# Kernel optimization log

Measured on AMD Instinct MI355X. Metric: run time of the kernel, lower is better.

The kernel has to match this reference:

```python
import jax, jax.numpy as jnp
import numpy as np

NUM_HEADS = 12
HEAD_SIZE = 64
HIDDEN = NUM_HEADS * HEAD_SIZE  # 768
ONE_SIDED_WINDOW = 256          # attention_window 512 // 2
NEG = -10000.0


def setup_inputs() -> dict:
    key = jax.random.key(0)
    ks = jax.random.split(key, 16)
    B, W, E, H = 1, 2048, 128, HIDDEN
    std = 0.02
    def lin(kw, kb):
        return (jax.random.normal(kw, (H, H), jnp.float32) * std,
                jax.random.normal(kb, (H,), jnp.float32) * std)
    q_w, q_b = lin(ks[0], ks[1])
    k_w, k_b = lin(ks[2], ks[3])
    v_w, v_b = lin(ks[4], ks[5])
    w2e_w, w2e_b = lin(ks[6], ks[7])
    e2w_w, e2w_b = lin(ks[8], ks[9])
    e2e_w, e2e_b = lin(ks[10], ks[11])
    return {
        "word_hidden_states": jax.random.normal(ks[12], (B, W, H), jnp.float32),
        "entity_hidden_states": jax.random.normal(ks[13], (B, E, H), jnp.float32),
        "attention_mask": jnp.zeros((B, 1, 1, W + E), jnp.float32),
        "q_w": q_w, "q_b": q_b, "k_w": k_w, "k_b": k_b, "v_w": v_w, "v_b": v_b,
        "w2e_w": w2e_w, "w2e_b": w2e_b, "e2w_w": e2w_w, "e2w_b": e2w_b,
        "e2e_w": e2e_w, "e2e_b": e2e_b,
    }


def reference(word_hidden_states, entity_hidden_states, attention_mask,
              q_w, q_b, k_w, k_b, v_w, v_b,
              w2e_w, w2e_b, e2w_w, e2w_b, e2e_w, e2e_b):
    B, W, H = word_hidden_states.shape
    E = entity_hidden_states.shape[1]
    S = W + E

    def heads(x):  # [B, L, H] -> [B, nh, L, hd]
        return x.reshape(B, -1, NUM_HEADS, HEAD_SIZE).transpose(0, 2, 1, 3)

    concat = jnp.concatenate([word_hidden_states, entity_hidden_states], axis=1)
    k = heads(concat @ k_w + k_b)          # [B, nh, S, hd]
    v = heads(concat @ v_w + v_b)
    q_w2w = heads(word_hidden_states @ q_w + q_b)
    q_w2e = heads(word_hidden_states @ w2e_w + w2e_b)
    q_e2w = heads(entity_hidden_states @ e2w_w + e2w_b)
    q_e2e = heads(entity_hidden_states @ e2e_w + e2e_b)

    k_word, k_ent = k[:, :, :W], k[:, :, W:]

    # --- w2w: Longformer sliding-window QK^T, then _conversion to a dense
    # [B, nh, W, W] matrix with out-of-band entries set to -10000. ---
    w2w = jnp.einsum('bhid,bhjd->bhij', q_w2w, k_word)  # [B, nh, W, W]
    idx = jnp.arange(W)
    in_band = jnp.abs(idx[:, None] - idx[None, :]) <= ONE_SIDED_WINDOW  # [W, W]
    # diagonal mask: float_mask[j] (-10000 where attention_mask != 0) added
    # within the band (broadcast over heads / query positions)
    mask_words = attention_mask[:, 0, 0, :W]                # [B, W]
    float_mask = jnp.where(mask_words != 0.0, NEG, 0.0)     # [B, W]
    w2w = w2w + float_mask[:, None, None, :]
    # _conversion: out-of-band -> -10000; also exact zeros -> -10000 (source quirk)
    w2w = jnp.where(in_band[None, None] & (w2w != 0.0), w2w, NEG)

    # --- entity-aware dense blocks ---
    w2e = jnp.einsum('bhid,bhjd->bhij', q_w2e, k_ent)    # [B, nh, W, E]
    e2w = jnp.einsum('bhid,bhjd->bhij', q_e2w, k_word)   # [B, nh, E, W]
    e2e = jnp.einsum('bhid,bhjd->bhij', q_e2e, k_ent)    # [B, nh, E, E]

    word_scores = jnp.concatenate([w2w, w2e], axis=3)    # [B, nh, W, S]
    ent_scores = jnp.concatenate([e2w, e2e], axis=3)     # [B, nh, E, S]
    scores = jnp.concatenate([word_scores, ent_scores], axis=2)  # [B, nh, S, S]

    scores = scores / jnp.sqrt(jnp.float32(HEAD_SIZE)) + attention_mask
    probs = jax.nn.softmax(scores, axis=-1)

    ctx = jnp.einsum('bhij,bhjd->bhid', probs, v)        # [B, nh, S, hd]
    ctx = ctx.transpose(0, 2, 1, 3).reshape(B, S, H)
    return ctx[:, :W, :], ctx[:, W:, :]
```

## Files before the change

kernel.cpp:

```cpp
#include <hip/hip_runtime.h>

typedef __bf16 bf16x8 __attribute__((ext_vector_type(8)));
typedef unsigned short u16x8 __attribute__((ext_vector_type(8)));
typedef u16x8 u16x8_a __attribute__((may_alias));
typedef unsigned int u32x2 __attribute__((ext_vector_type(2)));
typedef u32x2 u32x2_a __attribute__((may_alias));
typedef unsigned int u32x4 __attribute__((ext_vector_type(4)));
typedef u32x4 u32x4_a __attribute__((may_alias));
typedef float f32x4 __attribute__((ext_vector_type(4)));
typedef float f32x16 __attribute__((ext_vector_type(16)));

#define LOG2E 1.4426950408889634f
#define NEGV  -10000.0f

__device__ __forceinline__ unsigned int cvtpk(float lo, float hi){
  unsigned int r;
  asm("v_cvt_pk_bf16_f32 %0, %1, %2" : "=v"(r) : "v"(lo), "v"(hi));
  return r;
}
__device__ __forceinline__ bf16x8 ldb(const unsigned short* p){
  return __builtin_bit_cast(bf16x8, *(const u16x8_a*)p);
}
__device__ __forceinline__ bf16x8 mkfrag(unsigned a, unsigned b, unsigned c, unsigned d){
  u32x4 v = {a,b,c,d};
  return __builtin_bit_cast(bf16x8, v);
}
__device__ __forceinline__ void gload16(const unsigned short* g, unsigned short* l){
  __builtin_amdgcn_global_load_lds(
    (const __attribute__((address_space(1))) void*)g,
    (__attribute__((address_space(3))) void*)l, 16, 0, 0);
}

__global__ __launch_bounds__(256) void prep(
    const float* __restrict__ w0, const float* __restrict__ w1,
    const float* __restrict__ w2, const float* __restrict__ w3,
    const float* __restrict__ w4, const float* __restrict__ w5,
    const float* __restrict__ word, const float* __restrict__ ent,
    const float* __restrict__ am,
    unsigned short* __restrict__ outT, unsigned short* __restrict__ Abf,
    float* __restrict__ amT, float* __restrict__ negT)
{
  int z = blockIdx.z, tid = threadIdx.x;
  if (z == 6){
    size_t id = (size_t)blockIdx.y*24 + blockIdx.x;
    size_t e = (id*256 + tid)*8;
    const size_t WE = (size_t)2048*768;
    const float* s = (e < WE) ? (word + e) : (ent + (e - WE));
    float4 a = *(const float4*)s;
    float4 b = *(const float4*)(s+4);
    u32x4 v = {cvtpk(a.x,a.y), cvtpk(a.z,a.w), cvtpk(b.x,b.y), cvtpk(b.z,b.w)};
    *(u32x4_a*)(Abf + e) = v;
    return;
  }
  if (z == 7){
    if (blockIdx.y != 0 || blockIdx.x >= 9) return;
    int j = blockIdx.x*256 + tid;
    if (j < 2176){
      float a = am[j];
      amT[j]  = a * LOG2E;
      negT[j] = (a != 0.f) ? NEGV : 0.f;
    }
    return;
  }
  if (blockIdx.y >= 24) return;
  const float* src;
  switch (z){
    case 0: src = w0; break; case 1: src = w1; break; case 2: src = w2; break;
    case 3: src = w3; break; case 4: src = w4; break; default: src = w5; break;
  }
  unsigned short* dst = outT + (size_t)z * 589824;
  __shared__ float tile[32][33];
  int tx = tid & 31, ty = tid >> 5;
  int x0 = blockIdx.x*32, y0 = blockIdx.y*32;
  #pragma unroll
  for (int i=0;i<32;i+=8) tile[ty+i][tx] = src[(size_t)(y0+ty+i)*768 + x0+tx];
  __syncthreads();
  #pragma unroll
  for (int i=0;i<32;i+=16){
    unsigned int u = cvtpk(tile[tx][ty+i], tile[tx][ty+i+8]);
    dst[(size_t)(x0+ty+i)*768 + y0+tx]   = (unsigned short)u;
    dst[(size_t)(x0+ty+i+8)*768 + y0+tx] = (unsigned short)(u>>16);
  }
}

__global__ __launch_bounds__(256) void gemm_proj(
    const unsigned short* __restrict__ Abf,
    const unsigned short* __restrict__ wT,
    const float* __restrict__ bK, const float* __restrict__ bV,
    const float* __restrict__ bQ, const float* __restrict__ bWE,
    const float* __restrict__ bEW, const float* __restrict__ bEE,
    unsigned short* __restrict__ oK, unsigned short* __restrict__ VbT,
    unsigned short* __restrict__ oQ, unsigned short* __restrict__ oWE,
    unsigned short* __restrict__ oEW, unsigned short* __restrict__ oEE)
{
  int mt = blockIdx.x, ntile = blockIdx.y;
  int g, mg;
  if      (mt < 17){ g=0; mg=mt;    }
  else if (mt < 34){ g=1; mg=mt-17; }
  else if (mt < 50){ g=2; mg=mt-34; }
  else if (mt < 66){ g=3; mg=mt-50; }
  else if (mt < 67){ g=4; mg=0;     }
  else             { g=5; mg=0;     }
  int m0 = mg*128;
  const unsigned short* A = Abf + (size_t)((g>=4 ? 2048 : 0) + m0)*768;
  const unsigned short* B = wT + (size_t)g*589824;
  const float* bias; unsigned short* out;
  switch (g){
    case 0: bias=bK;  out=oK;  break;
    case 1: bias=bV;  out=0;   break;
    case 2: bias=bQ;  out=oQ;  break;
    case 3: bias=bWE; out=oWE; break;
    case 4: bias=bEW; out=oEW; break;
    default:bias=bEE; out=oEE; break;
  }
  int n0 = ntile*128;

  __shared__ __align__(16) unsigned short a_s[128*32];
  __shared__ __align__(16) unsigned short b_s[128*32];

  int tid  = threadIdx.x;
  int w    = tid>>6, lane = tid&63, quad = lane>>4, lr = lane&15;
  int wm   = (w&1)*64, wn = (w>>1)*64;

  f32x4 acc[4][4];
  #pragma unroll
  for (int i=0;i<4;i++) for (int j=0;j<4;j++) for (int r=0;r<4;r++) acc[i][j][r]=0.f;

  int srow = lane>>2;
  int scol = (lane&3)*8;
  const unsigned short* gA0 = A + (size_t)(w*32 + srow)*768 + scol;
  const unsigned short* gA1 = gA0 + (size_t)16*768;
  const unsigned short* gB0 = B + (size_t)(n0 + w*32 + srow)*768 + scol;
  const unsigned short* gB1 = gB0 + (size_t)16*768;
  unsigned short* lA0 = a_s + w*32*32;
  unsigned short* lA1 = lA0 + 16*32;
  unsigned short* lB0 = b_s + w*32*32;
  unsigned short* lB1 = lB0 + 16*32;

  for (int k0=0; k0<768; k0+=32){
    __syncthreads();
    gload16(gA0 + k0, lA0);
    gload16(gA1 + k0, lA1);
    gload16(gB0 + k0, lB0);
    gload16(gB1 + k0, lB1);
    __syncthreads();
    bf16x8 af[4], bfr[4];
    #pragma unroll
    for (int i=0;i<4;i++) af[i]  = ldb(a_s + (wm+i*16+lr)*32 + quad*8);
    #pragma unroll
    for (int j=0;j<4;j++) bfr[j] = ldb(b_s + (wn+j*16+lr)*32 + quad*8);
    #pragma unroll
    for (int i=0;i<4;i++)
      #pragma unroll
      for (int j=0;j<4;j++)
        acc[i][j] = __builtin_amdgcn_mfma_f32_16x16x32_bf16(af[i], bfr[j], acc[i][j], 0,0,0);
  }
  if (g == 1){
    #pragma unroll
    for (int j=0;j<4;j++){
      int col = n0 + wn + j*16 + lr;
      float bb = bias[col];
      #pragma unroll
      for (int i=0;i<4;i++){
        int rowb = m0 + wm + i*16 + quad*4;
        u32x2 uv = {cvtpk(acc[i][j][0]+bb, acc[i][j][1]+bb),
                    cvtpk(acc[i][j][2]+bb, acc[i][j][3]+bb)};
        *(u32x2_a*)(VbT + (size_t)col*2176 + rowb) = uv;
      }
    }
  } else {
    out += (size_t)m0*768;
    #pragma unroll
    for (int j=0;j<4;j++){
      int col = n0 + wn + j*16 + lr;
      float bb = bias[col];
      #pragma unroll
      for (int i=0;i<4;i++){
        int rowb = wm + i*16 + quad*4;
        unsigned int u01 = cvtpk(acc[i][j][0]+bb, acc[i][j][1]+bb);
        unsigned int u23 = cvtpk(acc[i][j][2]+bb, acc[i][j][3]+bb);
        out[(size_t)(rowb+0)*768 + col] = (unsigned short)u01;
        out[(size_t)(rowb+1)*768 + col] = (unsigned short)(u01>>16);
        out[(size_t)(rowb+2)*768 + col] = (unsigned short)u23;
        out[(size_t)(rowb+3)*768 + col] = (unsigned short)(u23>>16);
      }
    }
  }
}

__global__ __launch_bounds__(256) void attn_split(
  const unsigned short* __restrict__ Kb,  const unsigned short* __restrict__ VbT,
  const unsigned short* __restrict__ Qw,  const unsigned short* __restrict__ Qwe,
  const unsigned short* __restrict__ Qew, const unsigned short* __restrict__ Qee,
  const float* __restrict__ amT, const float* __restrict__ negT,
  float* __restrict__ outw, float* __restrict__ pO, float* __restrict__ pML)
{
  int lin = blockIdx.x + 80*blockIdx.y;
  int wid = (lin & 7)*120 + (lin >> 3);
  int bx = wid % 80;
  int h  = wid / 80;

  int tid = threadIdx.x, w = tid>>6, lane = tid&63;
  int l31 = lane & 31, hi = lane >> 5;
  int hi8 = hi*8, hi4 = hi*4;
  bool isword = bx < 64;
  int qrb, eg=0, eq=0;
  const unsigned short *Qa, *Qb;
  if (isword){ qrb = bx*32; Qa=Qw;  Qb=Qwe; }
  else       { int e = bx-64; eg = e>>2; eq = e&3; qrb = eg*32; Qa=Qew; Qb=Qee; }
  int hofs = h*64;

  __shared__ float part[4][64][35];

  const unsigned short* qr = Qa + (size_t)(qrb+l31)*768 + hofs + hi8;
  bf16x8 qa0 = ldb(qr), qa1 = ldb(qr+16), qa2 = ldb(qr+32), qa3 = ldb(qr+48);
  qr = Qb + (size_t)(qrb+l31)*768 + hofs + hi8;
  bf16x8 qb0 = ldb(qr), qb1 = ldb(qr+16), qb2 = ldb(qr+32), qb3 = ldb(qr+48);

  float m = -1e30f, l = 0.f;
  f32x16 o0, o1;
  #pragma unroll
  for (int r=0;r<16;r++){ o0[r] = 0.f; o1[r] = 0.f; }

  int lo, nw, start, end;
  if (isword){
    lo = qrb - 256; if (lo < 0) lo = 0;
    int hiq = qrb + 288; if (hiq > 2048) hiq = 2048;
    nw = (hiq - lo) >> 5;
    start = w; end = nw + 4;
  } else {
    lo = 0; nw = 64;
    start = eq*17 + w; end = eq*17 + 17;
  }
  int iq = qrb + l31;

  for (int c = start; c < end; c += 4){
    bool entp = c >= nw;
    int j0 = entp ? (2048 + (c-nw)*32) : (lo + c*32);

    const unsigned short* kp = Kb + (size_t)(j0+l31)*768 + hofs + hi8;
    bf16x8 ka0 = ldb(kp), ka1 = ldb(kp+16), ka2 = ldb(kp+32), ka3 = ldb(kp+48);
    const unsigned short* vp = VbT + (size_t)(hofs + l31)*2176 + j0 + hi8;
    bf16x8 va00 = ldb(vp),           va01 = ldb(vp + 16);
    bf16x8 va10 = ldb(vp + 32*2176), va11 = ldb(vp + 32*2176 + 16);
    float4 aT0 = *(const float4*)(amT + j0 + hi4);
    float4 aT1 = *(const float4*)(amT + j0 + 8  + hi4);
    float4 aT2 = *(const float4*)(amT + j0 + 16 + hi4);
    float4 aT3 = *(const float4*)(amT + j0 + 24 + hi4);

    bf16x8 qf0 = entp ? qb0 : qa0, qf1 = entp ? qb1 : qa1;
    bf16x8 qf2 = entp ? qb2 : qa2, qf3 = entp ? qb3 : qa3;

    f32x16 s;
    #pragma unroll
    for (int r=0;r<16;r++) s[r] = 0.f;
    __builtin_amdgcn_s_setprio(1);
    s = __builtin_amdgcn_mfma_f32_32x32x16_bf16(ka0, qf0, s, 0,0,0);
    s = __builtin_amdgcn_mfma_f32_32x32x16_bf16(ka1, qf1, s, 0,0,0);
    s = __builtin_amdgcn_mfma_f32_32x32x16_bf16(ka2, qf2, s, 0,0,0);
    s = __builtin_amdgcn_mfma_f32_32x32x16_bf16(ka3, qf3, s, 0,0,0);
    __builtin_amdgcn_s_setprio(0);

    float sc[16];
    if (isword && !entp){
      float4 nT0 = *(const float4*)(negT + j0 + hi4);
      float4 nT1 = *(const float4*)(negT + j0 + 8  + hi4);
      float4 nT2 = *(const float4*)(negT + j0 + 16 + hi4);
      float4 nT3 = *(const float4*)(negT + j0 + 24 + hi4);
      int djb = iq + 256 - (j0 + hi4);
      #pragma unroll
      for (int e=0;e<4;e++){
        { float sv = s[e]    + nT0[e];
          bool ok = ((unsigned)(djb - e)      <= 512u) && (sv != 0.f);
          sc[e]    = (ok ? sv : NEGV) * (LOG2E*0.125f) + aT0[e]; }
        { float sv = s[4+e]  + nT1[e];
          bool ok = ((unsigned)(djb - 8 - e)  <= 512u) && (sv != 0.f);
          sc[4+e]  = (ok ? sv : NEGV) * (LOG2E*0.125f) + aT1[e]; }
        { float sv = s[8+e]  + nT2[e];
          bool ok = ((unsigned)(djb - 16 - e) <= 512u) && (sv != 0.f);
          sc[8+e]  = (ok ? sv : NEGV) * (LOG2E*0.125f) + aT2[e]; }
        { float sv = s[12+e] + nT3[e];
          bool ok = ((unsigned)(djb - 24 - e) <= 512u) && (sv != 0.f);
          sc[12+e] = (ok ? sv : NEGV) * (LOG2E*0.125f) + aT3[e]; }
      }
    } else {
      #pragma unroll
      for (int e=0;e<4;e++){
        sc[e]    = s[e]    * (LOG2E*0.125f) + aT0[e];
        sc[4+e]  = s[4+e]  * (LOG2E*0.125f) + aT1[e];
        sc[8+e]  = s[8+e]  * (LOG2E*0.125f) + aT2[e];
        sc[12+e] = s[12+e] * (LOG2E*0.125f) + aT3[e];
      }
    }

    float mx = sc[0];
    #pragma unroll
    for (int r=1;r<16;r++) mx = fmaxf(mx, sc[r]);
    mx = fmaxf(mx, __shfl_xor(mx, 32));

    float mn;
    if (__all(mx <= m)){
      mn = m;
    } else {
      mn = fmaxf(m, mx);
      float alpha = exp2f(m - mn);
      m = mn;
      l *= alpha;
      #pragma unroll
      for (int r=0;r<16;r++){ o0[r] *= alpha; o1[r] *= alpha; }
    }

    float p[16];
    #pragma unroll
    for (int r=0;r<16;r++) p[r] = exp2f(sc[r]-mn);

    float rs = ((p[0]+p[1])+(p[2]+p[3])) + ((p[4]+p[5])+(p[6]+p[7]))
             + ((p[8]+p[9])+(p[10]+p[11])) + ((p[12]+p[13])+(p[14]+p[15]));
    rs += __shfl_xor(rs, 32);
    l += rs;

    unsigned pk0 = cvtpk(p[0], p[1]),  pk1 = cvtpk(p[2], p[3]);
    unsigned pk2 = cvtpk(p[4], p[5]),  pk3 = cvtpk(p[6], p[7]);
    unsigned pk4 = cvtpk(p[8], p[9]),  pk5 = cvtpk(p[10], p[11]);
    unsigned pk6 = cvtpk(p[12], p[13]),pk7 = cvtpk(p[14], p[15]);

    bool hib = hi != 0;
    unsigned t0 = hib ? pk0 : pk2;
    unsigned t1 = hib ? pk1 : pk3;
    unsigned t2 = hib ? pk4 : pk6;
    unsigned t3 = hib ? pk5 : pk7;
    unsigned r0 = (unsigned)__shfl_xor((int)t0, 32);
    unsigned r1 = (unsigned)__shfl_xor((int)t1, 32);
    unsigned r2 = (unsigned)__shfl_xor((int)t2, 32);
    unsigned r3 = (unsigned)__shfl_xor((int)t3, 32);
    bf16x8 pf1 = hib ? mkfrag(r0, r1, pk2, pk3) : mkfrag(pk0, pk1, r0, r1);
    bf16x8 pf2 = hib ? mkfrag(r2, r3, pk6, pk7) : mkfrag(pk4, pk5, r2, r3);

    __builtin_amdgcn_s_setprio(1);
    o0 = __builtin_amdgcn_mfma_f32_32x32x16_bf16(va00, pf1, o0, 0,0,0);
    o0 = __builtin_amdgcn_mfma_f32_32x32x16_bf16(va01, pf2, o0, 0,0,0);
    o1 = __builtin_amdgcn_mfma_f32_32x32x16_bf16(va10, pf1, o1, 0,0,0);
    o1 = __builtin_amdgcn_mfma_f32_32x32x16_bf16(va11, pf2, o1, 0,0,0);
    __builtin_amdgcn_s_setprio(0);
  }

  {
    float* my = &part[w][lane][0];
    my[0] = m; my[1] = l;
    #pragma unroll
    for (int r=0;r<16;r++){ my[2+r] = o0[r]; my[18+r] = o1[r]; }
  }
  __syncthreads();

  float mm[4], ll[4], e4[4];
  #pragma unroll
  for (int p=0;p<4;p++){ mm[p] = part[p][lane][0]; ll[p] = part[p][lane][1]; }
  float M = fmaxf(fmaxf(mm[0],mm[1]), fmaxf(mm[2],mm[3]));
  #pragma unroll
  for (int p=0;p<4;p++) e4[p] = exp2f(mm[p]-M);
  float L = ll[0]*e4[0] + ll[1]*e4[1] + ll[2]*e4[2] + ll[3]*e4[3];

  float mo0[4], mo1[4];
  #pragma unroll
  for (int k=0;k<4;k++){
    float a0 = 0.f, a1 = 0.f;
    #pragma unroll
    for (int p=0;p<4;p++){
      a0 += part[p][lane][2  + w*4 + k] * e4[p];
      a1 += part[p][lane][18 + w*4 + k] * e4[p];
    }
    mo0[k] = a0; mo1[k] = a1;
  }

  if (isword){
    float rinv = 1.f / L;
    float4 s0 = {mo0[0]*rinv, mo0[1]*rinv, mo0[2]*rinv, mo0[3]*rinv};
    float4 s1 = {mo1[0]*rinv, mo1[1]*rinv, mo1[2]*rinv, mo1[3]*rinv};
    float* ob = outw + (size_t)(qrb+l31)*768 + hofs + w*8 + hi4;
    *(float4*)(ob)      = s0;
    *(float4*)(ob + 32) = s1;
  } else {
    int idx = (eg*4 + eq)*12 + h;
    float* po = pO + (size_t)idx*2048 + l31*64 + w*8 + hi4;
    float4 s0 = {mo0[0], mo0[1], mo0[2], mo0[3]};
    float4 s1 = {mo1[0], mo1[1], mo1[2], mo1[3]};
    *(float4*)(po)      = s0;
    *(float4*)(po + 32) = s1;
    if (w == 0 && lane < 32){
      float* pml = pML + (size_t)idx*64;
      pml[lane*2]     = M;
      pml[lane*2 + 1] = L;
    }
  }
}

__global__ __launch_bounds__(256) void merge_ent(
    const float* __restrict__ pO, const float* __restrict__ pML,
    float* __restrict__ oute)
{
  int b = blockIdx.x;
  int eg = b/12, h = b%12;
  int tid = threadIdx.x;
  int row = tid>>3, cg = (tid&7)*8;
  float mq[4], lq[4];
  #pragma unroll
  for (int q=0;q<4;q++){
    int idx = (eg*4 + q)*12 + h;
    mq[q] = pML[(size_t)idx*64 + row*2];
    lq[q] = pML[(size_t)idx*64 + row*2 + 1];
  }
  float M = fmaxf(fmaxf(mq[0],mq[1]), fmaxf(mq[2],mq[3]));
  float L = 0.f, eqv[4];
  #pragma unroll
  for (int q=0;q<4;q++){ eqv[q] = exp2f(mq[q]-M); L += lq[q]*eqv[q]; }
  float rl = 1.f/L;
  float4 a0 = {0,0,0,0}, a1 = {0,0,0,0};
  #pragma unroll
  for (int q=0;q<4;q++){
    int idx = (eg*4 + q)*12 + h;
    const float* src = pO + (size_t)idx*2048 + row*64 + cg;
    float4 x = *(const float4*)(src);
    float4 y = *(const float4*)(src + 4);
    a0.x += x.x*eqv[q]; a0.y += x.y*eqv[q]; a0.z += x.z*eqv[q]; a0.w += x.w*eqv[q];
    a1.x += y.x*eqv[q]; a1.y += y.y*eqv[q]; a1.z += y.z*eqv[q]; a1.w += y.w*eqv[q];
  }
  a0.x*=rl; a0.y*=rl; a0.z*=rl; a0.w*=rl;
  a1.x*=rl; a1.y*=rl; a1.z*=rl; a1.w*=rl;
  float* dst = oute + (size_t)(eg*32+row)*768 + h*64 + cg;
  *(float4*)(dst)   = a0;
  *(float4*)(dst+4) = a1;
}

extern "C" void kernel_launch(void* const* d_in, const int* in_sizes, int n_in,
                              void* d_out, int out_size, void* d_ws, size_t ws_size,
                              hipStream_t stream) {
  const float* word  = (const float*)d_in[0];
  const float* ent   = (const float*)d_in[1];
  const float* am    = (const float*)d_in[2];
  const float* q_w   = (const float*)d_in[3];
  const float* q_b   = (const float*)d_in[4];
  const float* k_w   = (const float*)d_in[5];
  const float* k_b   = (const float*)d_in[6];
  const float* v_w   = (const float*)d_in[7];
  const float* v_b   = (const float*)d_in[8];
  const float* w2e_w = (const float*)d_in[9];
  const float* w2e_b = (const float*)d_in[10];
  const float* e2w_w = (const float*)d_in[11];
  const float* e2w_b = (const float*)d_in[12];
  const float* e2e_w = (const float*)d_in[13];
  const float* e2e_b = (const float*)d_in[14];

  unsigned short* ws  = (unsigned short*)d_ws;
  unsigned short* wT  = ws;
  unsigned short* Kb  = wT  + (size_t)6*589824;
  unsigned short* Tb  = Kb  + (size_t)2176*768;
  unsigned short* Qw  = Tb  + (size_t)2176*768;
  unsigned short* Qwe = Qw  + (size_t)2048*768;
  unsigned short* Qew = Qwe + (size_t)2048*768;
  unsigned short* Qee = Qew + (size_t)128*768;
  unsigned short* VbT = Qee + (size_t)128*768;
  unsigned short* Abf = VbT + (size_t)768*2176;

  float* amT  = (float*)Tb;
  float* negT = amT + 2176;

  float* pO  = (float*)wT;
  float* pML = pO + (size_t)192*2048;

  float* outw = (float*)d_out;
  float* oute = outw + (size_t)2048*768;

  hipLaunchKernelGGL(prep, dim3(24,34,8), dim3(256), 0, stream,
                     k_w, v_w, q_w, w2e_w, e2w_w, e2e_w, word, ent, am,
                     wT, Abf, amT, negT);
  hipLaunchKernelGGL(gemm_proj, dim3(68,6), dim3(256), 0, stream,
                     Abf, wT, k_b, v_b, q_b, w2e_b, e2w_b, e2e_b,
                     Kb, VbT, Qw, Qwe, Qew, Qee);
  hipLaunchKernelGGL(attn_split, dim3(80,12), dim3(256), 0, stream,
                     Kb, VbT, Qw, Qwe, Qew, Qee, amT, negT, outw, pO, pML);
  hipLaunchKernelGGL(merge_ent, dim3(48), dim3(256), 0, stream,
                     pO, pML, oute);
}
```

Baseline: 152.9 us.

## Halve projection GEMM M-tile and double-buffer LDS staging

The projection GEMM now uses 64x128 tiles instead of 128x128, doubling the grid from 68x6 to 136x6 blocks so more CUs are occupied. The K loop is double-buffered in LDS: the next K-slice is loaded while MFMAs run on the current one, leaving one barrier per iteration instead of two. The cost is more LDS per block, B tiles re-read by twice as many blocks, and a smaller MFMA-to-load ratio per wave.

After: 154.1 us. Within noise of the previous version (+0.8%).

```diff
diff --git a/kernel.cpp b/kernel.cpp
--- a/kernel.cpp
+++ b/kernel.cpp
@@ -95,13 +95,13 @@
 {
   int mt = blockIdx.x, ntile = blockIdx.y;
   int g, mg;
-  if      (mt < 17){ g=0; mg=mt;    }
-  else if (mt < 34){ g=1; mg=mt-17; }
-  else if (mt < 50){ g=2; mg=mt-34; }
-  else if (mt < 66){ g=3; mg=mt-50; }
-  else if (mt < 67){ g=4; mg=0;     }
-  else             { g=5; mg=0;     }
-  int m0 = mg*128;
+  if      (mt <  34){ g=0; mg=mt;     }
+  else if (mt <  68){ g=1; mg=mt-34;  }
+  else if (mt < 100){ g=2; mg=mt-68;  }
+  else if (mt < 132){ g=3; mg=mt-100; }
+  else if (mt < 134){ g=4; mg=mt-132; }
+  else              { g=5; mg=mt-134; }
+  int m0 = mg*64;
   const unsigned short* A = Abf + (size_t)((g>=4 ? 2048 : 0) + m0)*768;
   const unsigned short* B = wT + (size_t)g*589824;
   const float* bias; unsigned short* out;
@@ -115,53 +115,56 @@
   }
   int n0 = ntile*128;
 
-  __shared__ __align__(16) unsigned short a_s[128*32];
-  __shared__ __align__(16) unsigned short b_s[128*32];
+  __shared__ __align__(16) unsigned short a_s[2*64*32];
+  __shared__ __align__(16) unsigned short b_s[2*128*32];
 
   int tid  = threadIdx.x;
   int w    = tid>>6, lane = tid&63, quad = lane>>4, lr = lane&15;
-  int wm   = (w&1)*64, wn = (w>>1)*64;
-
-  f32x4 acc[4][4];
-  #pragma unroll
-  for (int i=0;i<4;i++) for (int j=0;j<4;j++) for (int r=0;r<4;r++) acc[i][j][r]=0.f;
+  int wm   = (w&1)*32, wn = (w>>1)*64;
+
+  f32x4 acc[2][4];
+  #pragma unroll
+  for (int i=0;i<2;i++) for (int j=0;j<4;j++) for (int r=0;r<4;r++) acc[i][j][r]=0.f;
 
   int srow = lane>>2;
   int scol = (lane&3)*8;
-  const unsigned short* gA0 = A + (size_t)(w*32 + srow)*768 + scol;
-  const unsigned short* gA1 = gA0 + (size_t)16*768;
+  const unsigned short* gA  = A + (size_t)(w*16 + srow)*768 + scol;
   const unsigned short* gB0 = B + (size_t)(n0 + w*32 + srow)*768 + scol;
   const unsigned short* gB1 = gB0 + (size_t)16*768;
-  unsigned short* lA0 = a_s + w*32*32;
-  unsigned short* lA1 = lA0 + 16*32;
-  unsigned short* lB0 = b_s + w*32*32;
-  unsigned short* lB1 = lB0 + 16*32;
-
+
+#define STAGE(BUF, K) do { \
+    gload16(gA  + (K), a_s + (BUF)*2048 + w*16*32); \
+    gload16(gB0 + (K), b_s + (BUF)*4096 + w*32*32); \
+    gload16(gB1 + (K), b_s + (BUF)*4096 + w*32*32 + 16*32); \
+  } while(0)
+
+  STAGE(0, 0);
+  __syncthreads();
+  int cur = 0;
   for (int k0=0; k0<768; k0+=32){
-    __syncthreads();
-    gload16(gA0 + k0, lA0);
-    gload16(gA1 + k0, lA1);
-    gload16(gB0 + k0, lB0);
-    gload16(gB1 + k0, lB1);
-    __syncthreads();
-    bf16x8 af[4], bfr[4];
-    #pragma unroll
-    for (int i=0;i<4;i++) af[i]  = ldb(a_s + (wm+i*16+lr)*32 + quad*8);
-    #pragma unroll
-    for (int j=0;j<4;j++) bfr[j] = ldb(b_s + (wn+j*16+lr)*32 + quad*8);
-    #pragma unroll
-    for (int i=0;i<4;i++)
+    if (k0 < 736) STAGE(cur^1, k0+32);
+    bf16x8 af[2], bfr[4];
+    #pragma unroll
+    for (int i=0;i<2;i++) af[i]  = ldb(a_s + cur*2048 + (wm+i*16+lr)*32 + quad*8);
+    #pragma unroll
+    for (int j=0;j<4;j++) bfr[j] = ldb(b_s + cur*4096 + (wn+j*16+lr)*32 + quad*8);
+    #pragma unroll
+    for (int i=0;i<2;i++)
       #pragma unroll
       for (int j=0;j<4;j++)
         acc[i][j] = __builtin_amdgcn_mfma_f32_16x16x32_bf16(af[i], bfr[j], acc[i][j], 0,0,0);
-  }
+    __syncthreads();
+    cur ^= 1;
+  }
+#undef STAGE
+
   if (g == 1){
     #pragma unroll
     for (int j=0;j<4;j++){
       int col = n0 + wn + j*16 + lr;
       float bb = bias[col];
       #pragma unroll
-      for (int i=0;i<4;i++){
+      for (int i=0;i<2;i++){
         int rowb = m0 + wm + i*16 + quad*4;
         u32x2 uv = {cvtpk(acc[i][j][0]+bb, acc[i][j][1]+bb),
                     cvtpk(acc[i][j][2]+bb, acc[i][j][3]+bb)};
@@ -175,7 +178,7 @@
       int col = n0 + wn + j*16 + lr;
       float bb = bias[col];
       #pragma unroll
-      for (int i=0;i<4;i++){
+      for (int i=0;i<2;i++){
         int rowb = wm + i*16 + quad*4;
         unsigned int u01 = cvtpk(acc[i][j][0]+bb, acc[i][j][1]+bb);
         unsigned int u23 = cvtpk(acc[i][j][2]+bb, acc[i][j][3]+bb);
@@ -473,7 +476,7 @@
   hipLaunchKernelGGL(prep, dim3(24,34,8), dim3(256), 0, stream,
                      k_w, v_w, q_w, w2e_w, e2w_w, e2e_w, word, ent, am,
                      wT, Abf, amT, negT);
-  hipLaunchKernelGGL(gemm_proj, dim3(68,6), dim3(256), 0, stream,
+  hipLaunchKernelGGL(gemm_proj, dim3(136,6), dim3(256), 0, stream,
                      Abf, wT, k_b, v_b, q_b, w2e_b, e2w_b, e2e_b,
                      Kb, VbT, Qw, Qwe, Qew, Qee);
   hipLaunchKernelGGL(attn_split, dim3(80,12), dim3(256), 0, stream,
```
